# Kernel optimization log

Measured on AMD Instinct MI355X. Metric: run time of the kernel, lower is better.

The kernel has to match this reference:

```python
import jax, jax.numpy as jnp
import numpy as np

B, N, D = 4, 4096, 1024
H = 16
HD = D // H            # 64 head dim
M = 256                # num random features
LN_EPS = 1e-5
KERNEL_EPS = 1e-4


def _gaussian_orthogonal_matrix(rng, num_rows, num_cols):
    """FAVOR+ orthogonal random projection, scaling=0 (row-norm multipliers)."""
    blocks = []
    n_full = num_rows // num_cols
    for _ in range(n_full):
        g = rng.standard_normal((num_cols, num_cols))
        q, _ = np.linalg.qr(g)
        blocks.append(q.T)
    rem = num_rows - n_full * num_cols
    if rem > 0:
        g = rng.standard_normal((num_cols, num_cols))
        q, _ = np.linalg.qr(g)
        blocks.append(q.T[:rem])
    mat = np.concatenate(blocks, axis=0)
    # scaling == 0: multiplier = row norms of an unstructured gaussian matrix
    multiplier = np.linalg.norm(rng.standard_normal((num_rows, num_cols)), axis=1)
    return (multiplier[:, None] * mat).astype(np.float32)


def favor_features(data, proj, is_query):
    """Nonnegative softmax kernel features. data: [B,H,N,HD], proj: [M,HD]."""
    d = data.shape[-1]
    data_normalizer = d ** -0.25
    ratio = proj.shape[0] ** -0.5
    data_dash = jnp.einsum('bhnd,md->bhnm', data_normalizer * data, proj)
    diag = 0.5 * (data_normalizer ** 2) * jnp.sum(data * data, axis=-1, keepdims=True)
    if is_query:
        mx = jnp.max(data_dash, axis=-1, keepdims=True)
    else:
        mx = jnp.max(data_dash, axis=(-1, -2), keepdims=True)
    return ratio * (jnp.exp(data_dash - diag - mx) + KERNEL_EPS)


def layer_norm(x, g, b):
    mu = jnp.mean(x, axis=-1, keepdims=True)
    var = jnp.mean((x - mu) ** 2, axis=-1, keepdims=True)
    return (x - mu) * jax.lax.rsqrt(var + LN_EPS) * g + b


def setup_inputs() -> dict:
    key = jax.random.key(0)
    ks = jax.random.split(key, 16)
    s_d = (1.0 / np.sqrt(D)).astype('float32') if False else 1.0 / np.sqrt(D)
    def lin(k, fin, fout):
        kw, kb = jax.random.split(k)
        lim = 1.0 / np.sqrt(fin)
        w = jax.random.uniform(kw, (fin, fout), jnp.float32, -lim, lim)
        b = jax.random.uniform(kb, (fout,), jnp.float32, -lim, lim)
        return w, b
    wq, bq = lin(ks[0], D, D)
    wk, bk = lin(ks[1], D, D)
    wv, bv = lin(ks[2], D, D)
    wo, bo = lin(ks[3], D, D)
    w1, b1 = lin(ks[4], D, 4 * D)
    w2, b2 = lin(ks[5], 4 * D, D)
    proj = jnp.asarray(_gaussian_orthogonal_matrix(np.random.default_rng(0), M, HD))
    x = jax.random.normal(ks[6], (B, N, D), jnp.float32)
    return dict(
        x=x, wq=wq, bq=bq, wk=wk, bk=bk, wv=wv, bv=bv, wo=wo, bo=bo,
        proj=proj, w1=w1, b1=b1, w2=w2, b2=b2,
        ln1_g=jnp.ones((D,), jnp.float32), ln1_b=jnp.zeros((D,), jnp.float32),
        ln2_g=jnp.ones((D,), jnp.float32), ln2_b=jnp.zeros((D,), jnp.float32),
    )


def reference(x, wq, bq, wk, bk, wv, bv, wo, bo, proj, w1, b1, w2, b2,
              ln1_g, ln1_b, ln2_g, ln2_b):
    def split_heads(t):  # [B,N,D] -> [B,H,N,HD]
        return t.reshape(B, N, H, HD).transpose(0, 2, 1, 3)

    residual = x
    Q = split_heads(x @ wq + bq)
    K = split_heads(x @ wk + bk)
    V = split_heads(x @ wv + bv)

    Qp = favor_features(Q, proj, is_query=True)    # [B,H,N,M]
    Kp = favor_features(K, proj, is_query=False)   # [B,H,N,M]

    # linear attention: Q' (K'^T V), O(N*M*HD)
    kv = jnp.einsum('bhnm,bhnd->bhmd', Kp, V)
    attn = jnp.einsum('bhnm,bhmd->bhnd', Qp, kv)
    denom = jnp.einsum('bhnm,bhm->bhn', Qp, jnp.sum(Kp, axis=2))
    attn = attn / denom[..., None]

    attn = attn.transpose(0, 2, 1, 3).reshape(B, N, D)
    x = attn @ wo + bo
    x = layer_norm(x + residual, ln1_g, ln1_b)

    residual = x
    h = jax.nn.gelu(x @ w1 + b1, approximate=False)
    x = h @ w2 + b2
    x = layer_norm(x + residual, ln2_g, ln2_b)
    return x
```

## Files before the change

kernel.cpp:

```cpp
#include <hip/hip_runtime.h>
#include <math.h>

#define DEV __device__ __forceinline__

typedef __attribute__((ext_vector_type(8))) short frag8;
typedef __attribute__((ext_vector_type(4))) float facc4;
typedef __attribute__((ext_vector_type(4))) unsigned short us4;
typedef __attribute__((ext_vector_type(8))) unsigned short us8;

DEV float bf2f(unsigned short u){ union{unsigned i; float f;} x; x.i=((unsigned)u)<<16; return x.f; }
DEV unsigned short f2bf(float f){ union{float f; unsigned i;} x; x.f=f;
  return (unsigned short)((x.i + 0x7FFFu + ((x.i>>16)&1u))>>16); }

#define GLD16(g, l) __builtin_amdgcn_global_load_lds( \
    (const __attribute__((address_space(1))) void*)(g), \
    (__attribute__((address_space(3))) void*)(l), 16, 0, 0)

template<int ROWS>
DEV void stage_tile(const unsigned short* __restrict__ g0, int ld, unsigned short* s0){
  static_assert(ROWS % 8 == 0, "");
  constexpr int SLOTS = ROWS/8;
  const int w = threadIdx.x>>6, lane = threadIdx.x&63;
  for (int s = w; s < SLOTS; s += 4) {
    int c  = (s<<6) + lane;
    int r  = c >> 3, cg = c & 7;
    int kg = cg ^ (r & 7);
    GLD16(g0 + (size_t)r*ld + (kg<<3), s0 + (s<<9));
  }
}

DEV frag8 frag_ld(const unsigned short* s, int row, int kg){
  int cg = kg ^ (row & 7);
  return *(const frag8*)(s + (row<<6) + (cg<<3));
}

template<int BM, int BN, int WR, int WC>
DEV void gemm_core(const unsigned short* __restrict__ Ag, int lda,
                   const unsigned short* __restrict__ Bg, int ldb,
                   int kIters, unsigned short* As, unsigned short* Bs,
                   facc4 (&acc)[BM/(WR*16)][BN/(WC*16)]) {
  constexpr int WM = BM/(WR*16), WN = BN/(WC*16);
  const int tid = threadIdx.x, w = tid>>6, lane = tid&63;
  const int wr = w / WC, wc = w % WC;
  const int col = lane & 15, quad = lane >> 4;
  for (int kt = 0; kt < kIters; ++kt) {
    stage_tile<BM>(Ag + kt*64, lda, As);
    stage_tile<BN>(Bg + kt*64, ldb, Bs);
    __syncthreads();
    #pragma unroll
    for (int ks = 0; ks < 2; ++ks) {
      frag8 af[WM], bfr[WN];
      #pragma unroll
      for (int i=0;i<WM;++i) af[i]  = frag_ld(As, wr*WM*16 + i*16 + col, ks*4+quad);
      #pragma unroll
      for (int j=0;j<WN;++j) bfr[j] = frag_ld(Bs, wc*WN*16 + j*16 + col, ks*4+quad);
      #pragma unroll
      for (int i=0;i<WM;++i)
        #pragma unroll
        for (int j=0;j<WN;++j)
          acc[i][j] = __builtin_amdgcn_mfma_f32_16x16x32_bf16(af[i], bfr[j], acc[i][j], 0,0,0);
    }
    __syncthreads();
  }
}

#define ZERO_ACC(acc, I, J) { facc4 zz = {0.f,0.f,0.f,0.f}; \
  _Pragma("unroll") for(int i_=0;i_<I;++i_) _Pragma("unroll") for(int j_=0;j_<J;++j_) acc[i_][j_]=zz; }

DEV void tr64(const float* __restrict__ in, unsigned short* __restrict__ out, int K, int N){
  __shared__ float t[64][65];
  const int bx = blockIdx.x*64, by = blockIdx.y*64;
  const int tid = threadIdx.x;
  const int r0 = tid>>4, c4 = (tid&15)*4;
  #pragma unroll
  for(int it=0; it<4; ++it){
    int r = r0 + it*16;
    float4 v = *(const float4*)(in + (size_t)(by+r)*N + bx + c4);
    t[r][c4+0]=v.x; t[r][c4+1]=v.y; t[r][c4+2]=v.z; t[r][c4+3]=v.w;
  }
  __syncthreads();
  #pragma unroll
  for(int it=0; it<4; ++it){
    int n = r0 + it*16;
    us4 o;
    #pragma unroll
    for(int e=0;e<4;++e) o[e] = f2bf(t[c4+e][n]);
    *(us4*)(out + (size_t)(bx+n)*K + by + c4) = o;
  }
}

__global__ void k_transpose4(const float* __restrict__ wq, const float* __restrict__ wk,
                             const float* __restrict__ wv, const float* __restrict__ wo,
                             unsigned short* __restrict__ wqkvT, unsigned short* __restrict__ woT){
  const float* in; unsigned short* out;
  int z = blockIdx.z;
  if(z==0){in=wq; out=wqkvT;} else if(z==1){in=wk; out=wqkvT+1048576;}
  else if(z==2){in=wv; out=wqkvT+2097152;} else {in=wo; out=woT;}
  tr64(in, out, 1024, 1024);
}

__global__ void k_transpose(const float* __restrict__ in, unsigned short* __restrict__ out,
                            int K, int N){ tr64(in, out, K, N); }

__global__ void k_misc(const float* __restrict__ x, unsigned short* __restrict__ xb,
                       const float* __restrict__ proj, unsigned short* __restrict__ projB,
                       unsigned short* __restrict__ Vt){
  int bx = blockIdx.x, tid = threadIdx.x;
  if(bx < 16384){
    int i = bx*256 + tid;
    float4 v = ((const float4*)x)[i];
    us4 o = {f2bf(v.x),f2bf(v.y),f2bf(v.z),f2bf(v.w)};
    ((us4*)xb)[i]=o;
  } else if(bx < 16400){
    int i = (bx-16384)*256 + tid;
    if(i<4096){ float4 v = ((const float4*)proj)[i];
      us4 o = {f2bf(v.x),f2bf(v.y),f2bf(v.z),f2bf(v.w)};
      ((us4*)projB)[i]=o; }
  } else {
    int i = (bx-16400)*256 + tid;
    int head=i>>12, n=i&4095;
    Vt[((size_t)head*80+64)*4096 + n] = 0x3F80;
  }
}

__global__ __launch_bounds__(256,2) void k_qkv(const unsigned short* __restrict__ xb,
    const unsigned short* __restrict__ wqkvT,
    const float* __restrict__ bq, const float* __restrict__ bk, const float* __restrict__ bv,
    unsigned short* __restrict__ Qb, unsigned short* __restrict__ Kb, unsigned short* __restrict__ Vt){
  __shared__ __align__(16) unsigned short As[128*64];
  __shared__ __align__(16) unsigned short Bs[128*64];
  facc4 acc[4][4]; ZERO_ACC(acc,4,4)
  const int bm = blockIdx.x, bn = blockIdx.y;
  gemm_core<128,128,2,2>(xb + (size_t)bm*128*1024, 1024,
                         wqkvT + (size_t)bn*128*1024, 1024, 16, As, Bs, acc);
  const int tid=threadIdx.x, w=tid>>6, lane=tid&63, col=lane&15, quad=lane>>4;
  const int wr=w>>1, wc=w&1;
  #pragma unroll
  for(int i=0;i<4;++i){
    int row0 = bm*128 + wr*64 + i*16 + quad*4;
    int bb = row0 >> 12, n0 = row0 & 4095;
    #pragma unroll
    for(int j=0;j<4;++j){
      int c = bn*128 + wc*64 + j*16 + col;
      int region = c >> 10, f = c & 1023, he = f >> 6, hd = f & 63;
      const float* bias = (region==0)? bq : (region==1)? bk : bv;
      float bsv = bias[f];
      if(region < 2){
        unsigned short* dst = (region==0? Qb : Kb) + ((size_t)(bb*16+he)*4096 + n0)*64 + hd;
        #pragma unroll
        for(int r=0;r<4;++r) dst[(size_t)r*64] = f2bf(acc[i][j][r] + bsv);
      } else {
        us4 pk;
        #pragma unroll
        for(int r=0;r<4;++r) pk[r] = f2bf(acc[i][j][r] + bsv);
        *(us4*)(Vt + ((size_t)(bb*16+he)*80 + hd)*4096 + n0) = pk;
      }
    }
  }
}

__global__ __launch_bounds__(256,2) void k_featq(const unsigned short* __restrict__ Qb,
    const unsigned short* __restrict__ projB, unsigned short* __restrict__ Qp, int qbase){
  __shared__ __align__(16) unsigned short As[128*64];
  __shared__ __align__(16) unsigned short Bs[256*64];
  __shared__ float diagS[128];
  __shared__ float maxS[128][2];
  facc4 acc[4][8]; ZERO_ACC(acc,4,8)
  const int br = blockIdx.x;
  gemm_core<128,256,2,2>(Qb + ((size_t)qbase*65536 + (size_t)br*128)*64, 64,
                         projB, 64, 1, As, Bs, acc);
  const int tid=threadIdx.x, w=tid>>6, lane=tid&63, col=lane&15, quad=lane>>4;
  const int wr=w>>1, wc=w&1;
  if(tid<128){ float ss=0.f;
    #pragma unroll
    for(int kg=0;kg<8;++kg){ frag8 v = frag_ld(As, tid, kg);
      #pragma unroll
      for(int e=0;e<8;++e){ float f=bf2f((unsigned short)v[e]); ss+=f*f; } }
    diagS[tid]=0.0625f*ss; }
  #pragma unroll
  for(int i=0;i<4;++i)
    #pragma unroll
    for(int r=0;r<4;++r){
      float m=-1e30f;
      #pragma unroll
      for(int j=0;j<8;++j) m=fmaxf(m,acc[i][j][r]);
      #pragma unroll
      for(int d=1;d<16;d<<=1) m=fmaxf(m,__shfl_xor(m,d));
      if(col==0) maxS[wr*64+i*16+quad*4+r][wc]=m;
    }
  __syncthreads();
  const float dn=0.35355339059327378f;
  unsigned short* Ct = Bs;
  size_t tokbase = (size_t)br*128;
  #pragma unroll
  for(int p=0;p<2;++p){
    if(wr==p){
      #pragma unroll
      for(int i=0;i<4;++i)
        #pragma unroll
        for(int r=0;r<4;++r){
          int tl = i*16+quad*4+r;
          int tf = p*64+tl;
          float dsub = diagS[tf] + dn*fmaxf(maxS[tf][0],maxS[tf][1]);
          #pragma unroll
          for(int j=0;j<8;++j){
            int m = wc*128 + j*16 + col;
            float val = 0.0625f*(__expf(dn*acc[i][j][r] - dsub) + 1e-4f);
            int cc = m>>3;
            Ct[tl*256 + ((cc ^ (tl&31))<<3) + (m&7)] = f2bf(val);
          }
        }
    }
    __syncthreads();
    for(int c=tid;c<2048;c+=256){
      int tl=c>>5, part=c&31;
      us8 v = *(const us8*)(Ct + tl*256 + ((part ^ (tl&31))<<3));
      *(us8*)(Qp + (tokbase + p*64 + tl)*256 + part*8) = v;
    }
    __syncthreads();
  }
}

__global__ __launch_bounds__(256,2) void k_fkmax(const unsigned short* __restrict__ Kb,
    const unsigned short* __restrict__ projB, float* __restrict__ pmax){
  __shared__ __align__(16) unsigned short As[128*64];
  __shared__ __align__(16) unsigned short Bs[256*64];
  __shared__ float wm[4];
  facc4 acc[4][8]; ZERO_ACC(acc,4,8)
  const int br = blockIdx.x;
  gemm_core<128,256,2,2>(Kb + (size_t)br*8192, 64, projB, 64, 1, As, Bs, acc);
  const int w=threadIdx.x>>6, lane=threadIdx.x&63;
  float m=-1e30f;
  #pragma unroll
  for(int i=0;i<4;++i)
    #pragma unroll
    for(int j=0;j<8;++j)
      #pragma unroll
      for(int r=0;r<4;++r) m=fmaxf(m, acc[i][j][r]);
  #pragma unroll
  for(int d=1; d<64; d<<=1) m=fmaxf(m, __shfl_xor(m,d));
  if(lane==0) wm[w]=m;
  __syncthreads();
  if(threadIdx.x==0)
    pmax[br] = fmaxf(fmaxf(wm[0],wm[1]),fmaxf(wm[2],wm[3])) * 0.35355339059327378f;
}

__global__ void k_mxk(const float* __restrict__ pmax, float* __restrict__ mxK){
  int h = threadIdx.x;
  float m=-1e30f;
  for(int i=0;i<32;++i) m=fmaxf(m, pmax[h*32+i]);
  mxK[h]=m;
}

__global__ __launch_bounds__(256,2) void k_featk(const unsigned short* __restrict__ Kb,
    const unsigned short* __restrict__ projB, const float* __restrict__ mxK,
    unsigned short* __restrict__ KpT, int qbase){
  __shared__ __align__(16) unsigned short As[128*64];
  __shared__ __align__(16) unsigned short Bs[256*64];
  __shared__ float diagS[128];
  facc4 acc[4][8]; ZERO_ACC(acc,4,8)
  const int br = blockIdx.x;
  gemm_core<128,256,2,2>(Kb + ((size_t)qbase*65536 + (size_t)br*128)*64, 64,
                         projB, 64, 1, As, Bs, acc);
  const int tid=threadIdx.x, w=tid>>6, lane=tid&63, col=lane&15, quad=lane>>4;
  const int wr=w>>1, wc=w&1;
  if(tid<128){ float ss=0.f;
    #pragma unroll
    for(int kg=0;kg<8;++kg){ frag8 v = frag_ld(As, tid, kg);
      #pragma unroll
      for(int e=0;e<8;++e){ float f=bf2f((unsigned short)v[e]); ss+=f*f; } }
    diagS[tid]=0.0625f*ss; }
  __syncthreads();
  const int lh = br>>5, n0 = (br&31)*128;
  const float mxh = mxK[qbase*16 + lh];
  const float dn=0.35355339059327378f;
  unsigned short* Ct = Bs;
  #pragma unroll
  for(int p=0;p<2;++p){
    if(wc==p){
      #pragma unroll
      for(int i=0;i<4;++i)
        #pragma unroll
        for(int r=0;r<4;++r){
          int tok = wr*64 + i*16 + quad*4 + r;
          float dsub = diagS[tok] + mxh;
          int tc = tok>>3;
          #pragma unroll
          for(int j=0;j<8;++j){
            int ml = j*16 + col;
            float val = 0.0625f*(__expf(dn*acc[i][j][r] - dsub) + 1e-4f);
            Ct[ml*128 + ((tc ^ (ml&15))<<3) + (tok&7)] = f2bf(val);
          }
        }
    }
    __syncthreads();
    for(int c=tid;c<2048;c+=256){
      int ml=c>>4, part=c&15;
      us8 v = *(const us8*)(Ct + ml*128 + ((part ^ (ml&15))<<3));
      *(us8*)(KpT + ((size_t)(lh*256 + p*128 + ml))*4096 + n0 + part*8) = v;
    }
    __syncthreads();
  }
}

__global__ __launch_bounds__(256,2) void k_kv(const unsigned short* __restrict__ KpT,
    const unsigned short* __restrict__ Vt, float* __restrict__ part, int qbase){
  __shared__ __align__(16) unsigned short As[256*64];
  __shared__ __align__(16) unsigned short Bs[80*64];
  facc4 acc[4][5]; ZERO_ACC(acc,4,5)
  const int ksp = blockIdx.x, lh = blockIdx.y;
  gemm_core<256,80,4,1>(KpT + (size_t)lh*1048576 + ksp*256, 4096,
                        Vt  + ((size_t)(qbase*16+lh))*327680 + ksp*256, 4096, 4, As, Bs, acc);
  const int w=threadIdx.x>>6, lane=threadIdx.x&63, col=lane&15, quad=lane>>4;
  #pragma unroll
  for(int i=0;i<4;++i){
    int mp0 = w*64 + i*16 + quad*4;
    #pragma unroll
    for(int j=0;j<5;++j){
      int d = j*16+col;
      *(facc4*)(part + (((size_t)(ksp*16 + lh))*80 + d)*256 + mp0) = acc[i][j];
    }
  }
}

__global__ void k_kvred(const float* __restrict__ part, unsigned short* __restrict__ kvT, int qbase){
  int i = blockIdx.x*256 + threadIdx.x;
  float4 s = {0.f,0.f,0.f,0.f};
  #pragma unroll
  for(int ks=0;ks<16;++ks){ float4 v = ((const float4*)part)[(size_t)ks*81920 + i];
    s.x+=v.x; s.y+=v.y; s.z+=v.z; s.w+=v.w; }
  us4 o = {f2bf(s.x),f2bf(s.y),f2bf(s.z),f2bf(s.w)};
  ((us4*)kvT)[(size_t)qbase*81920 + i] = o;
}

__global__ __launch_bounds__(256,2) void k_attn(const unsigned short* __restrict__ Qp,
    const unsigned short* __restrict__ kvT, unsigned short* __restrict__ attnOut, int qbase){
  __shared__ __align__(16) unsigned short As[128*64];
  __shared__ __align__(16) unsigned short Bs[80*64];
  facc4 acc[2][5]; ZERO_ACC(acc,2,5)
  const int mb = blockIdx.x, lh = blockIdx.y;
  gemm_core<128,80,4,1>(Qp  + (size_t)lh*1048576 + (size_t)mb*32768, 256,
                        kvT + ((size_t)(qbase*16+lh))*20480, 256, 4, As, Bs, acc);
  const int w=threadIdx.x>>6, lane=threadIdx.x&63, col=lane&15, quad=lane>>4;
  const int gh = qbase*16 + lh, b = gh>>4, h = gh&15;
  unsigned short* Ct = As;
  #pragma unroll
  for(int i=0;i<2;++i)
    #pragma unroll
    for(int r=0;r<4;++r){
      float den = __shfl(acc[i][4][r], lane & 48);
      float inv = 1.0f/den;
      int tok = w*32 + i*16 + quad*4 + r;
      #pragma unroll
      for(int j=0;j<4;++j){
        int hd = j*16 + col;
        int cc = hd>>3;
        Ct[tok*64 + ((cc ^ (tok&7))<<3) + (hd&7)] = f2bf(acc[i][j][r]*inv);
      }
    }
  __syncthreads();
  const int n0 = mb*128;
  for(int c=threadIdx.x;c<1024;c+=256){
    int row=c>>3, part=c&7;
    us8 v = *(const us8*)(Ct + row*64 + ((part ^ (row&7))<<3));
    *(us8*)(attnOut + ((size_t)(b*4096) + n0 + row)*1024 + h*64 + part*8) = v;
  }
}

__global__ __launch_bounds__(256,2) void k_oproj(const unsigned short* __restrict__ attnOut,
    const unsigned short* __restrict__ woT, const float* __restrict__ bo,
    const float* __restrict__ x, unsigned short* __restrict__ y1){
  __shared__ __align__(16) unsigned short As[128*64];
  __shared__ __align__(16) unsigned short Bs[128*64];
  facc4 acc[4][4]; ZERO_ACC(acc,4,4)
  const int bm = blockIdx.x, bn = blockIdx.y;
  gemm_core<128,128,2,2>(attnOut + (size_t)bm*128*1024, 1024,
                         woT + (size_t)bn*128*1024, 1024, 16, As, Bs, acc);
  const int tid=threadIdx.x, w=tid>>6, lane=tid&63, col=lane&15, quad=lane>>4;
  const int wr=w>>1, wc=w&1;
  #pragma unroll
  for(int i=0;i<4;++i){
    int row0 = bm*128 + wr*64 + i*16 + quad*4;
    #pragma unroll
    for(int j=0;j<4;++j){
      int c = bn*128 + wc*64 + j*16 + col;
      float bsv = bo[c];
      #pragma unroll
      for(int r=0;r<4;++r){
        size_t idx = (size_t)(row0+r)*1024 + c;
        y1[idx] = f2bf(acc[i][j][r] + bsv + x[idx]);
      }
    }
  }
}

__global__ __launch_bounds__(256,2) void k_ffn1(const unsigned short* __restrict__ xb2,
    const unsigned short* __restrict__ w1T, const float* __restrict__ b1,
    unsigned short* __restrict__ hbuf, int hbase){
  __shared__ __align__(16) unsigned short As[128*64];
  __shared__ __align__(16) unsigned short Bs[128*64];
  facc4 acc[4][4]; ZERO_ACC(acc,4,4)
  const int bm = blockIdx.x, bn = blockIdx.y;
  gemm_core<128,128,2,2>(xb2 + ((size_t)(hbase*64 + bm))*131072, 1024,
                         w1T + (size_t)bn*128*1024, 1024, 16, As, Bs, acc);
  const int tid=threadIdx.x, w=tid>>6, lane=tid&63, col=lane&15, quad=lane>>4;
  const int wr=w>>1, wc=w&1;
  #pragma unroll
  for(int i=0;i<4;++i){
    int lrow0 = bm*128 + wr*64 + i*16 + quad*4;
    #pragma unroll
    for(int j=0;j<4;++j){
      int c = bn*128 + wc*64 + j*16 + col;
      float bsv = b1[c];
      #pragma unroll
      for(int r=0;r<4;++r){
        float v = acc[i][j][r] + bsv;
        float g = 0.5f*v*(1.0f+erff(v*0.70710678118654752f));
        hbuf[(size_t)(lrow0+r)*4096 + c] = f2bf(g);
      }
    }
  }
}

__global__ __launch_bounds__(256,2) void k_ffn2(const unsigned short* __restrict__ hbuf,
    const unsigned short* __restrict__ w2T, const float* __restrict__ b2,
    const unsigned short* __restrict__ xb2, unsigned short* __restrict__ y2, int hbase){
  __shared__ __align__(16) unsigned short As[128*64];
  __shared__ __align__(16) unsigned short Bs[128*64];
  facc4 acc[4][4]; ZERO_ACC(acc,4,4)
  const int bm = blockIdx.x, bn = blockIdx.y;
  gemm_core<128,128,2,2>(hbuf + (size_t)bm*128*4096, 4096,
                         w2T + (size_t)bn*128*4096, 4096, 64, As, Bs, acc);
  const int tid=threadIdx.x, w=tid>>6, lane=tid&63, col=lane&15, quad=lane>>4;
  const int wr=w>>1, wc=w&1;
  #pragma unroll
  for(int i=0;i<4;++i){
    int grow0 = hbase*8192 + bm*128 + wr*64 + i*16 + quad*4;
    #pragma unroll
    for(int j=0;j<4;++j){
      int c = bn*128 + wc*64 + j*16 + col;
      float bsv = b2[c];
      #pragma unroll
      for(int r=0;r<4;++r){
        size_t idx = (size_t)(grow0+r)*1024 + c;
        y2[idx] = f2bf(acc[i][j][r] + bsv + bf2f(xb2[idx]));
      }
    }
  }
}

__global__ __launch_bounds__(256) void k_lnb(const unsigned short* __restrict__ in,
    const float* __restrict__ g, const float* __restrict__ b,
    float* __restrict__ outf, unsigned short* __restrict__ outb){
  const int row = blockIdx.x*4 + (threadIdx.x>>6);
  const int lane = threadIdx.x&63;
  const unsigned short* x = in + (size_t)row*1024 + lane*16;
  float v[16];
  float s=0.f, s2=0.f;
  #pragma unroll
  for(int q=0;q<2;++q){ us8 u = *(const us8*)(x + q*8);
    #pragma unroll
    for(int e=0;e<8;++e){ float f=bf2f(u[e]); v[q*8+e]=f; s+=f; s2+=f*f; } }
  #pragma unroll
  for(int d=32;d;d>>=1){ s+=__shfl_xor(s,d); s2+=__shfl_xor(s2,d); }
  float mu = s*(1.0f/1024.0f), var = s2*(1.0f/1024.0f)-mu*mu;
  float rinv = rsqrtf(var+1e-5f);
  const int cb = lane*16;
  if(outf){
    #pragma unroll
    for(int q=0;q<4;++q){
      float4 o;
      o.x=(v[q*4+0]-mu)*rinv*g[cb+q*4+0]+b[cb+q*4+0];
      o.y=(v[q*4+1]-mu)*rinv*g[cb+q*4+1]+b[cb+q*4+1];
      o.z=(v[q*4+2]-mu)*rinv*g[cb+q*4+2]+b[cb+q*4+2];
      o.w=(v[q*4+3]-mu)*rinv*g[cb+q*4+3]+b[cb+q*4+3];
      *(float4*)(outf + (size_t)row*1024 + cb + q*4) = o;
    }
  }
  if(outb){
    #pragma unroll
    for(int q=0;q<2;++q){
      us8 o;
      #pragma unroll
      for(int e=0;e<8;++e) o[e]=f2bf((v[q*8+e]-mu)*rinv*g[cb+q*8+e]+b[cb+q*8+e]);
      *(us8*)(outb + (size_t)row*1024 + cb + q*8) = o;
    }
  }
}

extern "C" void kernel_launch(void* const* d_in, const int* in_sizes, int n_in,
                              void* d_out, int out_size, void* d_ws, size_t ws_size,
                              hipStream_t stream){
  const float* x   = (const float*)d_in[0];
  const float* wq  = (const float*)d_in[1];
  const float* bq  = (const float*)d_in[2];
  const float* wk  = (const float*)d_in[3];
  const float* bk  = (const float*)d_in[4];
  const float* wv  = (const float*)d_in[5];
  const float* bv  = (const float*)d_in[6];
  const float* wo  = (const float*)d_in[7];
  const float* bo  = (const float*)d_in[8];
  const float* proj= (const float*)d_in[9];
  const float* w1  = (const float*)d_in[10];
  const float* b1  = (const float*)d_in[11];
  const float* w2  = (const float*)d_in[12];
  const float* b2  = (const float*)d_in[13];
  const float* ln1g= (const float*)d_in[14];
  const float* ln1b= (const float*)d_in[15];
  const float* ln2g= (const float*)d_in[16];
  const float* ln2b= (const float*)d_in[17];
  (void)in_sizes; (void)n_in; (void)out_size;

  char* ws = (char*)d_ws;
  size_t off = 0;
  auto alloc = [&](size_t bytes)->char*{ char* p = ws + off; off += (bytes + 255) & ~(size_t)255; return p; };
  unsigned short* wqkvT = (unsigned short*)alloc(6291456);
  unsigned short* woT   = (unsigned short*)alloc(2097152);
  unsigned short* w1T   = (unsigned short*)alloc(8388608);
  unsigned short* w2T   = (unsigned short*)alloc(8388608);
  unsigned short* projB = (unsigned short*)alloc(32768);
  unsigned short* kvT   = (unsigned short*)alloc(2621440);
  float* pmax = (float*)alloc(16384);
  float* mxK  = (float*)alloc(256);
  char* R = alloc(230686720ull);
  if (off > ws_size) return;

  unsigned short* xb   = (unsigned short*)R;
  unsigned short* Qp   = (unsigned short*)R;
  unsigned short* Qb   = (unsigned short*)(R + 33554432);
  unsigned short* xb2  = (unsigned short*)(R + 33554432);
  unsigned short* Kb   = (unsigned short*)(R + 67108864);
  unsigned short* hbuf = (unsigned short*)(R + 67108864);
  unsigned short* Vt   = (unsigned short*)(R + 100663296);
  unsigned short* KpT  = (unsigned short*)(R + 142606336);
  float*          kvpart = (float*)(R + 176160768);
  unsigned short* attnOut = (unsigned short*)(R + 197132288);
  unsigned short* y2   = (unsigned short*)(R + 197132288);
  unsigned short* y1   = (unsigned short*)R;

  dim3 blk(256);
  k_transpose4<<<dim3(16,16,4),blk,0,stream>>>(wq, wk, wv, wo, wqkvT, woT);
  k_transpose<<<dim3(64,16),blk,0,stream>>>(w1, w1T, 1024, 4096);
  k_transpose<<<dim3(16,64),blk,0,stream>>>(w2, w2T, 4096, 1024);
  k_misc<<<17424,blk,0,stream>>>(x, xb, proj, projB, Vt);

  k_qkv<<<dim3(128,24),blk,0,stream>>>(xb, wqkvT, bq, bk, bv, Qb, Kb, Vt);
  k_fkmax<<<2048,blk,0,stream>>>(Kb, projB, pmax);
  k_mxk<<<1,64,0,stream>>>(pmax, mxK);

  for (int q = 0; q < 4; ++q) {
    k_featq<<<512,blk,0,stream>>>(Qb, projB, Qp, q);
    k_featk<<<512,blk,0,stream>>>(Kb, projB, mxK, KpT, q);
    k_kv<<<dim3(16,16),blk,0,stream>>>(KpT, Vt, kvpart, q);
    k_kvred<<<320,blk,0,stream>>>(kvpart, kvT, q);
    k_attn<<<dim3(32,16),blk,0,stream>>>(Qp, kvT, attnOut, q);
  }

  k_oproj<<<dim3(128,8),blk,0,stream>>>(attnOut, woT, bo, x, y1);
  k_lnb<<<4096,blk,0,stream>>>(y1, ln1g, ln1b, nullptr, xb2);

  for (int h = 0; h < 2; ++h) {
    k_ffn1<<<dim3(64,32),blk,0,stream>>>(xb2, w1T, b1, hbuf, h);
    k_ffn2<<<dim3(64,8),blk,0,stream>>>(hbuf, w2T, b2, xb2, y2, h);
  }
  k_lnb<<<4096,blk,0,stream>>>(y2, ln2g, ln2b, (float*)d_out, nullptr);
}
```

Before: 1.009 ms.

## Process all heads in one pass when workspace allows, removing chunk loops

When the workspace holds about 411MB, the code lays out buffers so that feature maps, KV and attention run over all 64 batch-heads in single launches, and the FFN runs in one pass instead of two halves. The k_kv and k_kvred kernels are generalised to take a variable K-split count and head count. This removes about 14 kernel launches and the small-grid tail effects of the quarter-sized launches. It needs a larger workspace and keeps the old chunked path as a fallback.

```diff
diff --git a/kernel.cpp b/kernel.cpp
--- a/kernel.cpp
+++ b/kernel.cpp
@@ -304,13 +304,14 @@
 }
 
 __global__ __launch_bounds__(256,2) void k_kv(const unsigned short* __restrict__ KpT,
-    const unsigned short* __restrict__ Vt, float* __restrict__ part, int qbase){
+    const unsigned short* __restrict__ Vt, float* __restrict__ part, int kiters){
   __shared__ __align__(16) unsigned short As[256*64];
   __shared__ __align__(16) unsigned short Bs[80*64];
   facc4 acc[4][5]; ZERO_ACC(acc,4,5)
-  const int ksp = blockIdx.x, lh = blockIdx.y;
-  gemm_core<256,80,4,1>(KpT + (size_t)lh*1048576 + ksp*256, 4096,
-                        Vt  + ((size_t)(qbase*16+lh))*327680 + ksp*256, 4096, 4, As, Bs, acc);
+  const int ksp = blockIdx.x, lh = blockIdx.y, heads = gridDim.y;
+  const int t0 = ksp*kiters*64;
+  gemm_core<256,80,4,1>(KpT + (size_t)lh*1048576 + t0, 4096,
+                        Vt  + (size_t)lh*327680  + t0, 4096, kiters, As, Bs, acc);
   const int w=threadIdx.x>>6, lane=threadIdx.x&63, col=lane&15, quad=lane>>4;
   #pragma unroll
   for(int i=0;i<4;++i){
@@ -318,19 +319,19 @@
     #pragma unroll
     for(int j=0;j<5;++j){
       int d = j*16+col;
-      *(facc4*)(part + (((size_t)(ksp*16 + lh))*80 + d)*256 + mp0) = acc[i][j];
-    }
-  }
-}
-
-__global__ void k_kvred(const float* __restrict__ part, unsigned short* __restrict__ kvT, int qbase){
+      *(facc4*)(part + (((size_t)(ksp*heads + lh))*80 + d)*256 + mp0) = acc[i][j];
+    }
+  }
+}
+
+__global__ void k_kvred(const float* __restrict__ part, unsigned short* __restrict__ kvT,
+                        int nsplit, int chunk){
   int i = blockIdx.x*256 + threadIdx.x;
   float4 s = {0.f,0.f,0.f,0.f};
-  #pragma unroll
-  for(int ks=0;ks<16;++ks){ float4 v = ((const float4*)part)[(size_t)ks*81920 + i];
+  for(int ks=0;ks<nsplit;++ks){ float4 v = ((const float4*)part)[(size_t)ks*chunk + i];
     s.x+=v.x; s.y+=v.y; s.z+=v.z; s.w+=v.w; }
   us4 o = {f2bf(s.x),f2bf(s.y),f2bf(s.z),f2bf(s.w)};
-  ((us4*)kvT)[(size_t)qbase*81920 + i] = o;
+  ((us4*)kvT)[i] = o;
 }
 
 __global__ __launch_bounds__(256,2) void k_attn(const unsigned short* __restrict__ Qp,
@@ -522,46 +523,68 @@
   unsigned short* kvT   = (unsigned short*)alloc(2621440);
   float* pmax = (float*)alloc(16384);
   float* mxK  = (float*)alloc(256);
-  char* R = alloc(230686720ull);
+
+  const bool full = (off + 411041792ull) <= ws_size;
+  char* R = alloc(full ? 411041792ull : 230686720ull);
   if (off > ws_size) return;
 
-  unsigned short* xb   = (unsigned short*)R;
-  unsigned short* Qp   = (unsigned short*)R;
-  unsigned short* Qb   = (unsigned short*)(R + 33554432);
-  unsigned short* xb2  = (unsigned short*)(R + 33554432);
-  unsigned short* Kb   = (unsigned short*)(R + 67108864);
-  unsigned short* hbuf = (unsigned short*)(R + 67108864);
-  unsigned short* Vt   = (unsigned short*)(R + 100663296);
-  unsigned short* KpT  = (unsigned short*)(R + 142606336);
-  float*          kvpart = (float*)(R + 176160768);
-  unsigned short* attnOut = (unsigned short*)(R + 197132288);
-  unsigned short* y2   = (unsigned short*)(R + 197132288);
-  unsigned short* y1   = (unsigned short*)R;
-
   dim3 blk(256);
+  unsigned short* xb = (unsigned short*)R;
+  unsigned short* Qb = (unsigned short*)(R + 33554432);
+  unsigned short* Kb = (unsigned short*)(R + 67108864);
+  unsigned short* Vt = (unsigned short*)(R + 100663296);
+
   k_transpose4<<<dim3(16,16,4),blk,0,stream>>>(wq, wk, wv, wo, wqkvT, woT);
   k_transpose<<<dim3(64,16),blk,0,stream>>>(w1, w1T, 1024, 4096);
   k_transpose<<<dim3(16,64),blk,0,stream>>>(w2, w2T, 4096, 1024);
   k_misc<<<17424,blk,0,stream>>>(x, xb, proj, projB, Vt);
-
   k_qkv<<<dim3(128,24),blk,0,stream>>>(xb, wqkvT, bq, bk, bv, Qb, Kb, Vt);
   k_fkmax<<<2048,blk,0,stream>>>(Kb, projB, pmax);
   k_mxk<<<1,64,0,stream>>>(pmax, mxK);
 
-  for (int q = 0; q < 4; ++q) {
-    k_featq<<<512,blk,0,stream>>>(Qb, projB, Qp, q);
-    k_featk<<<512,blk,0,stream>>>(Kb, projB, mxK, KpT, q);
-    k_kv<<<dim3(16,16),blk,0,stream>>>(KpT, Vt, kvpart, q);
-    k_kvred<<<320,blk,0,stream>>>(kvpart, kvT, q);
-    k_attn<<<dim3(32,16),blk,0,stream>>>(Qp, kvT, attnOut, q);
-  }
-
-  k_oproj<<<dim3(128,8),blk,0,stream>>>(attnOut, woT, bo, x, y1);
-  k_lnb<<<4096,blk,0,stream>>>(y1, ln1g, ln1b, nullptr, xb2);
-
-  for (int h = 0; h < 2; ++h) {
-    k_ffn1<<<dim3(64,32),blk,0,stream>>>(xb2, w1T, b1, hbuf, h);
-    k_ffn2<<<dim3(64,8),blk,0,stream>>>(hbuf, w2T, b2, xb2, y2, h);
-  }
-  k_lnb<<<4096,blk,0,stream>>>(y2, ln2g, ln2b, (float*)d_out, nullptr);
-}
+  if (full) {
+    unsigned short* Qp      = (unsigned short*)(R + 142606336);
+    unsigned short* KpT     = (unsigned short*)(R + 276824064);
+    float*          kvpart  = (float*)R;
+    unsigned short* attnOut = (unsigned short*)(R + 67108864);
+    unsigned short* y1      = (unsigned short*)R;
+    unsigned short* xb2     = (unsigned short*)(R + 33554432);
+    unsigned short* hbuf    = (unsigned short*)(R + 142606336);
+    unsigned short* y2      = (unsigned short*)(R + 100663296);
+
+    k_featq<<<2048,blk,0,stream>>>(Qb, projB, Qp, 0);
+    k_featk<<<2048,blk,0,stream>>>(Kb, projB, mxK, KpT, 0);
+    k_kv<<<dim3(8,64),blk,0,stream>>>(KpT, Vt, kvpart, 8);
+    k_kvred<<<1280,blk,0,stream>>>(kvpart, kvT, 8, 327680);
+    k_attn<<<dim3(32,64),blk,0,stream>>>(Qp, kvT, attnOut, 0);
+    k_oproj<<<dim3(128,8),blk,0,stream>>>(attnOut, woT, bo, x, y1);
+    k_lnb<<<4096,blk,0,stream>>>(y1, ln1g, ln1b, nullptr, xb2);
+    k_ffn1<<<dim3(128,32),blk,0,stream>>>(xb2, w1T, b1, hbuf, 0);
+    k_ffn2<<<dim3(128,8),blk,0,stream>>>(hbuf, w2T, b2, xb2, y2, 0);
+    k_lnb<<<4096,blk,0,stream>>>(y2, ln2g, ln2b, (float*)d_out, nullptr);
+  } else {
+    unsigned short* Qp      = (unsigned short*)R;
+    unsigned short* xb2     = (unsigned short*)(R + 33554432);
+    unsigned short* hbuf    = (unsigned short*)(R + 67108864);
+    unsigned short* KpT     = (unsigned short*)(R + 142606336);
+    float*          kvpart  = (float*)(R + 176160768);
+    unsigned short* attnOut = (unsigned short*)(R + 197132288);
+    unsigned short* y2      = (unsigned short*)(R + 197132288);
+    unsigned short* y1      = (unsigned short*)R;
+
+    for (int q = 0; q < 4; ++q) {
+      k_featq<<<512,blk,0,stream>>>(Qb, projB, Qp, q);
+      k_featk<<<512,blk,0,stream>>>(Kb, projB, mxK, KpT, q);
+      k_kv<<<dim3(16,16),blk,0,stream>>>(KpT, Vt + (size_t)q*16*327680, kvpart, 4);
+      k_kvred<<<320,blk,0,stream>>>(kvpart, kvT + (size_t)q*327680, 16, 81920);
+      k_attn<<<dim3(32,16),blk,0,stream>>>(Qp, kvT, attnOut, q);
+    }
+    k_oproj<<<dim3(128,8),blk,0,stream>>>(attnOut, woT, bo, x, y1);
+    k_lnb<<<4096,blk,0,stream>>>(y1, ln1g, ln1b, nullptr, xb2);
+    for (int h = 0; h < 2; ++h) {
+      k_ffn1<<<dim3(64,32),blk,0,stream>>>(xb2, w1T, b1, hbuf, h);
+      k_ffn2<<<dim3(64,8),blk,0,stream>>>(hbuf, w2T, b2, xb2, y2, h);
+    }
+    k_lnb<<<4096,blk,0,stream>>>(y2, ln2g, ln2b, (float*)d_out, nullptr);
+  }
+}
```

Measured after the change: 1.024 ms. Within noise of the previous version (+1.5%).
